# Performance work log

Measured on AMD Instinct MI355X. Metric: run time of the kernel, lower is better.

Reference implementation:

```python
import jax, jax.numpy as jnp
import numpy as np

B, C, H, W = 4, 256, 128, 128


def setup_inputs() -> dict:
    key = jax.random.key(0)
    k1, k2, k3, k4 = jax.random.split(key, 4)
    x = jax.random.normal(k1, (B, C, H, W), dtype=jnp.float32)
    offset = jax.random.normal(k2, (B, 18, H, W), dtype=jnp.float32)
    # 1x1 conv weights, normal_init std=0.01, zero bias (mmcv normal_init default)
    w0 = jax.random.normal(k3, (C, C), dtype=jnp.float32) * 0.01
    b0 = jnp.zeros((C,), dtype=jnp.float32)
    w1 = jax.random.normal(k4, (C, C), dtype=jnp.float32) * 0.01
    b1 = jnp.zeros((C,), dtype=jnp.float32)
    return {"x": x, "offset": offset, "w0": w0, "b0": b0, "w1": w1, "b1": b1}


def _bilinear(x, py, px):
    # x: [B,C,H,W]; py,px: [B,H,W] fractional sample coords; zero outside bounds (DCN convention)
    Bb, Cc, Hh, Ww = x.shape
    y0 = jnp.floor(py)
    x0 = jnp.floor(px)
    wy = (py - y0)[:, None]  # [B,1,H,W]
    wx = (px - x0)[:, None]
    y0i = y0.astype(jnp.int32)
    x0i = x0.astype(jnp.int32)
    xf = x.reshape(Bb, Cc, Hh * Ww)

    def corner(yi, xi):
        valid = ((yi >= 0) & (yi < Hh) & (xi >= 0) & (xi < Ww)).astype(x.dtype)
        idx = (jnp.clip(yi, 0, Hh - 1) * Ww + jnp.clip(xi, 0, Ww - 1)).reshape(Bb, 1, Hh * Ww)
        v = jnp.take_along_axis(xf, idx, axis=2).reshape(Bb, Cc, Hh, Ww)
        return v * valid[:, None]

    v00 = corner(y0i, x0i)
    v01 = corner(y0i, x0i + 1)
    v10 = corner(y0i + 1, x0i)
    v11 = corner(y0i + 1, x0i + 1)
    return (v00 * (1 - wy) * (1 - wx) + v01 * (1 - wy) * wx
            + v10 * wy * (1 - wx) + v11 * wy * wx)


def _channel_norm(t):
    t = t - t.mean(axis=1, keepdims=True)
    return t / jnp.sqrt(jnp.sum(t * t, axis=1, keepdims=True) + 1e-5)


def reference(x, offset, w0, b0, w1, b1):
    Bb, Cc, Hh, Ww = x.shape
    ys = jnp.arange(Hh, dtype=x.dtype)[:, None]  # [H,1]
    xs = jnp.arange(Ww, dtype=x.dtype)[None, :]  # [1,W]
    # deformable 3x3 unfold fused with max over the 9 sample points
    q = None
    for k in range(9):
        kh, kw = k // 3 - 1, k % 3 - 1
        py = ys + kh + offset[:, 2 * k]      # [B,H,W]
        px = xs + kw + offset[:, 2 * k + 1]
        s = _bilinear(x, py, px)             # [B,C,H,W]
        q = s if q is None else jnp.maximum(q, s)
    query = jnp.einsum('oc,bchw->bohw', w0, q) + b0[None, :, None, None]
    key = jnp.einsum('oc,bchw->bohw', w1, x) + b1[None, :, None, None]
    out = jnp.sum(_channel_norm(query) * _channel_norm(key), axis=1, keepdims=True)
    return out  # [B,1,H,W]
```

## Files before the change

kernel.cpp:

```cpp
#include <hip/hip_runtime.h>
#include <math.h>
#include <float.h>

#define Bd 4
#define Cd 256
#define Hd 128
#define Wd 128
#define HW (Hd*Wd)

#define PX 128
#define KC 32
#define PPW 8

#define PXT 64
#define CSTR 264

typedef __attribute__((ext_vector_type(8))) short s16x8;
typedef __attribute__((ext_vector_type(4))) float f32x4;

__device__ __forceinline__ void bf16split(float v, ushort& h, ushort& lo_) {
  uint u = __builtin_bit_cast(uint, v);
  uint uh = u + 0x7FFFu + ((u >> 16) & 1u);
  ushort hh = (ushort)(uh >> 16);
  float hf = __builtin_bit_cast(float, (uint)hh << 16);
  float res = v - hf;
  uint r = __builtin_bit_cast(uint, res);
  uint rl = r + 0x7FFFu + ((r >> 16) & 1u);
  h = hh; lo_ = (ushort)(rl >> 16);
}

__global__ __launch_bounds__(256) void prep_w_k(
    const float* __restrict__ w0, const float* __restrict__ w1,
    ushort* __restrict__ wpk) {
  const int t    = blockIdx.x * 256 + threadIdx.x;
  const int lane = t & 63;
  const int tile = (t >> 6) & 15;
  const int kc   = (t >> 10) & 7;
  const int mat  = t >> 13;
  const float* wsrc = mat ? w1 : w0;
  const int o  = tile * 16 + (lane & 15);
  const int c0 = kc * 32 + (lane >> 4) * 8;
  ushort hi[8], lo[8];
#pragma unroll
  for (int j = 0; j < 8; ++j)
    bf16split(wsrc[o * Cd + c0 + j], hi[j], lo[j]);
  const size_t bh = ((((size_t)(mat * 2 + 0) * 8 + kc) * 16 + tile) * 64 + lane) * 8;
  const size_t bl = ((((size_t)(mat * 2 + 1) * 8 + kc) * 16 + tile) * 64 + lane) * 8;
#pragma unroll
  for (int j = 0; j < 8; ++j) { wpk[bh + j] = hi[j]; wpk[bl + j] = lo[j]; }
}

__global__ __launch_bounds__(256) void transpose_x_k(
    const float* __restrict__ x, float* __restrict__ xT) {
  __shared__ float t[32][33];
  const int b   = blockIdx.z;
  const int hw0 = blockIdx.x * 32;
  const int c0  = blockIdx.y * 32;
  const int tx = threadIdx.x & 31, ty = threadIdx.x >> 5;
  const float* xb  = x  + (size_t)b * Cd * HW;
  float*       xTb = xT + (size_t)b * HW * Cd;
#pragma unroll
  for (int i = 0; i < 32; i += 8)
    t[ty + i][tx] = xb[(size_t)(c0 + ty + i) * HW + hw0 + tx];
  __syncthreads();
#pragma unroll
  for (int i = 0; i < 32; i += 8)
    xTb[(size_t)(hw0 + ty + i) * Cd + c0 + tx] = t[tx][ty + i];
}

__device__ __forceinline__ void deform_job(
    int j, int pbase, const float* __restrict__ offb, uint* __restrict__ dstbase) {
  const int px = j / 9, k = j - px * 9;
  const int p = pbase + px;
  const int h = p >> 7, w = p & (Wd - 1);
  const float oy = offb[(2 * k) * HW + p];
  const float ox = offb[(2 * k + 1) * HW + p];
  const float py = (float)(h + k / 3 - 1) + oy;
  const float pxx = (float)(w + k % 3 - 1) + ox;
  const float y0f = floorf(py), x0f = floorf(pxx);
  const float wy = py - y0f, wx = pxx - x0f;
  const int y0 = (int)y0f, x0 = (int)x0f;
  const int y1 = y0 + 1,  x1 = x0 + 1;
  const float vy0 = (y0 >= 0 && y0 < Hd) ? 1.f : 0.f;
  const float vy1 = (y1 >= 0 && y1 < Hd) ? 1.f : 0.f;
  const float vx0 = (x0 >= 0 && x0 < Wd) ? 1.f : 0.f;
  const float vx1 = (x1 >= 0 && x1 < Wd) ? 1.f : 0.f;
  const int cy0 = min(max(y0, 0), Hd-1), cy1 = min(max(y1, 0), Hd-1);
  const int cx0 = min(max(x0, 0), Wd-1), cx1 = min(max(x1, 0), Wd-1);
  uint4 iv;
  iv.x = (uint)(cy0 * Wd + cx0) * Cd;
  iv.y = (uint)(cy0 * Wd + cx1) * Cd;
  iv.z = (uint)(cy1 * Wd + cx0) * Cd;
  iv.w = (uint)(cy1 * Wd + cx1) * Cd;
  float4 cv;
  cv.x = (1.f-wy)*(1.f-wx) * vy0*vx0;
  cv.y = (1.f-wy)*wx       * vy0*vx1;
  cv.z = wy*(1.f-wx)       * vy1*vx0;
  cv.w = wy*wx             * vy1*vx1;
  uint* d = dstbase + (size_t)(px * 9 + k) * 8;
  *(uint4*)d = iv;
  *(float4*)(d + 4) = cv;
}

__global__ __launch_bounds__(256) void deform_coal_k(
    const float* __restrict__ xT, const float* __restrict__ off,
    float* __restrict__ qT) {
  __shared__ __align__(16) uint coef[4][PPW * 9 * 8];

  const int bid = blockIdx.x;
  const int swz = (bid & 7) * 256 + (bid >> 3);
  const int b    = swz >> 9;
  const int tile = swz & 511;

  const int wv    = threadIdx.x >> 6;
  const int lane  = threadIdx.x & 63;
  const int pbase = (tile * 4 + wv) * PPW;

  const float* offb = off + (size_t)b * 18 * HW;

  deform_job(lane, pbase, offb, &coef[wv][0]);
  if (lane < 8) deform_job(64 + lane, pbase, offb, &coef[wv][0]);
  __syncthreads();

  const float* xTb = xT + (size_t)b * HW * Cd + lane * 4;
  float*       qTb = qT + (size_t)b * HW * Cd + lane * 4;

#pragma unroll 2
  for (int pi = 0; pi < PPW; ++pi) {
    const int p = pbase + pi;
    float m0 = -FLT_MAX, m1 = -FLT_MAX, m2 = -FLT_MAX, m3 = -FLT_MAX;
#pragma unroll
    for (int k = 0; k < 9; ++k) {
      const uint* cp = &coef[wv][(pi * 9 + k) * 8];
      const uint4  iv = *(const uint4*)cp;
      const float4 cw = *(const float4*)(cp + 4);
      const float4 v00 = *(const float4*)(xTb + iv.x);
      const float4 v01 = *(const float4*)(xTb + iv.y);
      const float4 v10 = *(const float4*)(xTb + iv.z);
      const float4 v11 = *(const float4*)(xTb + iv.w);
      m0 = fmaxf(m0, fmaf(cw.x, v00.x, fmaf(cw.y, v01.x, fmaf(cw.z, v10.x, cw.w*v11.x))));
      m1 = fmaxf(m1, fmaf(cw.x, v00.y, fmaf(cw.y, v01.y, fmaf(cw.z, v10.y, cw.w*v11.y))));
      m2 = fmaxf(m2, fmaf(cw.x, v00.z, fmaf(cw.y, v01.z, fmaf(cw.z, v10.z, cw.w*v11.z))));
      m3 = fmaxf(m3, fmaf(cw.x, v00.w, fmaf(cw.y, v01.w, fmaf(cw.z, v10.w, cw.w*v11.w))));
    }
    float4 r; r.x = m0; r.y = m1; r.z = m2; r.w = m3;
    *(float4*)(qTb + (size_t)p * Cd) = r;
  }
}

__global__ __launch_bounds__(512) void fused_mfma_k(
    const float* __restrict__ xT, const float* __restrict__ qT,
    const ushort* __restrict__ wpk,
    const float* __restrict__ b0, const float* __restrict__ b1,
    float* __restrict__ out) {
  __shared__ ushort act[4 * PXT * CSTR];
  const int b   = blockIdx.y;
  const int px0 = blockIdx.x * PXT;
  const int tid = threadIdx.x;
  const int l   = tid & 63, wv = tid >> 6;

  {
    const int r  = tid >> 3;
    const int c0 = (tid & 7) * 32;
    const float* qrow = qT + ((size_t)b * HW + px0 + r) * Cd + c0;
    const float* xrow = xT + ((size_t)b * HW + px0 + r) * Cd + c0;
    ushort* dq_h = act + 0 * PXT * CSTR + r * CSTR + c0;
    ushort* dq_l = act + 1 * PXT * CSTR + r * CSTR + c0;
    ushort* dx_h = act + 2 * PXT * CSTR + r * CSTR + c0;
    ushort* dx_l = act + 3 * PXT * CSTR + r * CSTR + c0;
#pragma unroll
    for (int i = 0; i < 8; ++i) {
      const float4 qv = ((const float4*)qrow)[i];
      const float4 xv = ((const float4*)xrow)[i];
      ushort4 qh, ql, xh, xl;
      bf16split(qv.x, qh.x, ql.x); bf16split(qv.y, qh.y, ql.y);
      bf16split(qv.z, qh.z, ql.z); bf16split(qv.w, qh.w, ql.w);
      bf16split(xv.x, xh.x, xl.x); bf16split(xv.y, xh.y, xl.y);
      bf16split(xv.z, xh.z, xl.z); bf16split(xv.w, xh.w, xl.w);
      *(ushort4*)(dq_h + 4*i) = qh; *(ushort4*)(dq_l + 4*i) = ql;
      *(ushort4*)(dx_h + 4*i) = xh; *(ushort4*)(dx_l + 4*i) = xl;
    }
  }
  __syncthreads();

  const f32x4 z = {0.f, 0.f, 0.f, 0.f};
  f32x4 accQ[2][4], accK[2][4];
#pragma unroll
  for (int a = 0; a < 2; ++a)
#pragma unroll
    for (int bt = 0; bt < 4; ++bt) { accQ[a][bt] = z; accK[a][bt] = z; }

#pragma unroll 2
  for (int kc = 0; kc < 8; ++kc) {
    s16x8 a0h[2], a0l[2], a1h[2], a1l[2];
#pragma unroll
    for (int a = 0; a < 2; ++a) {
      const int tile = wv * 2 + a;
      a0h[a] = *(const s16x8*)(wpk + (((size_t)(0 * 8 + kc) * 16 + tile) * 64 + l) * 8);
      a0l[a] = *(const s16x8*)(wpk + (((size_t)(1 * 8 + kc) * 16 + tile) * 64 + l) * 8);
      a1h[a] = *(const s16x8*)(wpk + (((size_t)(2 * 8 + kc) * 16 + tile) * 64 + l) * 8);
      a1l[a] = *(const s16x8*)(wpk + (((size_t)(3 * 8 + kc) * 16 + tile) * 64 + l) * 8);
    }
#pragma unroll
    for (int bt = 0; bt < 4; ++bt) {
      const int row  = bt * 16 + (l & 15);
      const int coff = kc * 32 + (l >> 4) * 8;
      const ushort* base = act + row * CSTR + coff;
      const s16x8 bqh = *(const s16x8*)(base + 0 * PXT * CSTR);
      const s16x8 bql = *(const s16x8*)(base + 1 * PXT * CSTR);
      const s16x8 bxh = *(const s16x8*)(base + 2 * PXT * CSTR);
      const s16x8 bxl = *(const s16x8*)(base + 3 * PXT * CSTR);
#pragma unroll
      for (int a = 0; a < 2; ++a) {
        accQ[a][bt] = __builtin_amdgcn_mfma_f32_16x16x32_bf16(a0h[a], bqh, accQ[a][bt], 0, 0, 0);
        accQ[a][bt] = __builtin_amdgcn_mfma_f32_16x16x32_bf16(a0h[a], bql, accQ[a][bt], 0, 0, 0);
        accQ[a][bt] = __builtin_amdgcn_mfma_f32_16x16x32_bf16(a0l[a], bqh, accQ[a][bt], 0, 0, 0);
        accK[a][bt] = __builtin_amdgcn_mfma_f32_16x16x32_bf16(a1h[a], bxh, accK[a][bt], 0, 0, 0);
        accK[a][bt] = __builtin_amdgcn_mfma_f32_16x16x32_bf16(a1h[a], bxl, accK[a][bt], 0, 0, 0);
        accK[a][bt] = __builtin_amdgcn_mfma_f32_16x16x32_bf16(a1l[a], bxh, accK[a][bt], 0, 0, 0);
      }
    }
  }

  float bq[2][4], bk[2][4];
#pragma unroll
  for (int a = 0; a < 2; ++a)
#pragma unroll
    for (int r = 0; r < 4; ++r) {
      const int o = wv * 32 + a * 16 + (l >> 4) * 4 + r;
      bq[a][r] = b0[o]; bk[a][r] = b1[o];
    }

  float st[4][5];
#pragma unroll
  for (int bt = 0; bt < 4; ++bt)
#pragma unroll
    for (int s = 0; s < 5; ++s) st[bt][s] = 0.f;
#pragma unroll
  for (int bt = 0; bt < 4; ++bt)
#pragma unroll
    for (int a = 0; a < 2; ++a)
#pragma unroll
      for (int r = 0; r < 4; ++r) {
        const float Qv = accQ[a][bt][r] + bq[a][r];
        const float Kv = accK[a][bt][r] + bk[a][r];
        st[bt][0] += Qv;
        st[bt][1] += Kv;
        st[bt][2] = fmaf(Qv, Qv, st[bt][2]);
        st[bt][3] = fmaf(Kv, Kv, st[bt][3]);
        st[bt][4] = fmaf(Qv, Kv, st[bt][4]);
      }
#pragma unroll
  for (int bt = 0; bt < 4; ++bt)
#pragma unroll
    for (int s = 0; s < 5; ++s) {
      float v = st[bt][s];
      v += __shfl_xor(v, 16, 64);
      v += __shfl_xor(v, 32, 64);
      st[bt][s] = v;
    }

  __syncthreads();
  float* sl = (float*)act;
  {
    const int mybt = l >> 4, col = l & 15;
#pragma unroll
    for (int s = 0; s < 5; ++s)
      sl[((wv * 64) + mybt * 16 + col) * 5 + s] = st[mybt][s];
  }
  __syncthreads();
  if (tid < PXT) {
    float sQ = 0.f, sK = 0.f, sQQ = 0.f, sKK = 0.f, sQK = 0.f;
#pragma unroll
    for (int w8 = 0; w8 < 8; ++w8) {
      const float* p = sl + ((w8 * 64) + tid) * 5;
      sQ += p[0]; sK += p[1]; sQQ += p[2]; sKK += p[3]; sQK += p[4];
    }
    const float num = sQK - sQ * sK * (1.f / 256.f);
    const float dq  = sQQ - sQ * sQ * (1.f / 256.f) + 1e-5f;
    const float dk  = sKK - sK * sK * (1.f / 256.f) + 1e-5f;
    out[(size_t)b * HW + px0 + tid] = num / sqrtf(dq * dk);
  }
}

__global__ __launch_bounds__(256) void transpose_k(
    const float* __restrict__ w0, const float* __restrict__ w1,
    float* __restrict__ w0T, float* __restrict__ w1T) {
  __shared__ float tile[32][33];
  const float* src = blockIdx.y ? w1 : w0;
  float*       dst = blockIdx.y ? w1T : w0T;
  const int bx = blockIdx.x & 7, by = blockIdx.x >> 3;
  const int tx = threadIdx.x & 31, ty = threadIdx.x >> 5;
#pragma unroll
  for (int i = 0; i < 32; i += 8)
    tile[ty + i][tx] = src[(by*32 + ty + i)*Cd + bx*32 + tx];
  __syncthreads();
#pragma unroll
  for (int i = 0; i < 32; i += 8)
    dst[(bx*32 + ty + i)*Cd + by*32 + tx] = tile[tx][ty + i];
}

__global__ __launch_bounds__(256) void deform_max_k(
    const float* __restrict__ x, const float* __restrict__ off,
    float* __restrict__ q) {
  const int b   = blockIdx.y;
  const int c0  = blockIdx.z << 5;
  const int hw0 = (blockIdx.x << 8) + threadIdx.x;
  const int h   = hw0 >> 7;
  const int w   = hw0 & (Wd - 1);
  const float* offb = off + ((size_t)b * 18) * HW + hw0;
  int   i00[9], i01[9], i10[9], i11[9];
  float c00[9], c01[9], c10[9], c11[9];
#pragma unroll
  for (int k = 0; k < 9; ++k) {
    const int kh = k / 3 - 1, kw = k % 3 - 1;
    const float oy = offb[(size_t)(2*k)   * HW];
    const float ox = offb[(size_t)(2*k+1) * HW];
    const float py = (float)(h + kh) + oy;
    const float px = (float)(w + kw) + ox;
    const float y0f = floorf(py), x0f = floorf(px);
    const float wy = py - y0f, wx = px - x0f;
    const int y0 = (int)y0f, x0 = (int)x0f;
    const int y1 = y0 + 1,  x1 = x0 + 1;
    const float vy0 = (y0 >= 0 && y0 < Hd) ? 1.f : 0.f;
    const float vy1 = (y1 >= 0 && y1 < Hd) ? 1.f : 0.f;
    const float vx0 = (x0 >= 0 && x0 < Wd) ? 1.f : 0.f;
    const float vx1 = (x1 >= 0 && x1 < Wd) ? 1.f : 0.f;
    const int cy0 = min(max(y0, 0), Hd-1), cy1 = min(max(y1, 0), Hd-1);
    const int cx0 = min(max(x0, 0), Wd-1), cx1 = min(max(x1, 0), Wd-1);
    i00[k] = cy0 * Wd + cx0;  i01[k] = cy0 * Wd + cx1;
    i10[k] = cy1 * Wd + cx0;  i11[k] = cy1 * Wd + cx1;
    c00[k] = (1.f-wy)*(1.f-wx) * vy0*vx0;
    c01[k] = (1.f-wy)*wx       * vy0*vx1;
    c10[k] = wy*(1.f-wx)       * vy1*vx0;
    c11[k] = wy*wx             * vy1*vx1;
  }
  const float* xb = x + ((size_t)(b * Cd + c0)) * HW;
  float*       qb = q + ((size_t)(b * Cd + c0)) * HW + hw0;
#pragma unroll 4
  for (int c = 0; c < 32; ++c) {
    const float* xc = xb + (size_t)c * HW;
    float m = -3.402823466e38f;
#pragma unroll
    for (int k = 0; k < 9; ++k) {
      const float s = c00[k]*xc[i00[k]] + c01[k]*xc[i01[k]]
                    + c10[k]*xc[i10[k]] + c11[k]*xc[i11[k]];
      m = fmaxf(m, s);
    }
    qb[(size_t)c * HW] = m;
  }
}

__global__ __launch_bounds__(512) void fused_k(
    const float* __restrict__ x, const float* __restrict__ q,
    const float* __restrict__ w0T, const float* __restrict__ w1T,
    const float* __restrict__ b0, const float* __restrict__ b1,
    float* __restrict__ out) {
  __shared__ float w0s[KC * 256];
  __shared__ float w1s[KC * 256];
  __shared__ float qs [KC * PX];
  __shared__ float xs [KC * PX];
  const int b    = blockIdx.y;
  const int px0  = blockIdx.x * PX;
  const int tid  = threadIdx.x;
  const int o_t  = tid & 31;
  const int px_t = tid >> 5;
  float accQ[8][8], accK[8][8];
#pragma unroll
  for (int i = 0; i < 8; ++i) {
    const int o = (i < 4) ? (4*o_t + i) : (128 + 4*o_t + (i - 4));
    const float bqv = b0[o], bkv = b1[o];
#pragma unroll
    for (int j = 0; j < 8; ++j) { accQ[i][j] = bqv; accK[i][j] = bkv; }
  }
  const float* qb = q + ((size_t)b * Cd) * HW + px0;
  const float* xb = x + ((size_t)b * Cd) * HW + px0;
  for (int kc = 0; kc < Cd; kc += KC) {
    __syncthreads();
    {
      const float4* s0 = (const float4*)(w0T + (size_t)kc * 256);
      const float4* s1 = (const float4*)(w1T + (size_t)kc * 256);
      float4* d0 = (float4*)w0s;
      float4* d1 = (float4*)w1s;
#pragma unroll
      for (int i = 0; i < 4; ++i) {
        d0[tid*4 + i] = s0[tid*4 + i];
        d1[tid*4 + i] = s1[tid*4 + i];
      }
#pragma unroll
      for (int i = 0; i < 2; ++i) {
        const int f  = tid*2 + i;
        const int cc = f >> 5, p4 = f & 31;
        ((float4*)qs)[cc*(PX/4) + p4] =
            ((const float4*)(qb + (size_t)(kc+cc) * HW))[p4];
        ((float4*)xs)[cc*(PX/4) + p4] =
            ((const float4*)(xb + (size_t)(kc+cc) * HW))[p4];
      }
    }
    __syncthreads();
#pragma unroll 4
    for (int cc = 0; cc < KC; ++cc) {
      float a0[8], a1[8], qv[8], xv[8];
      *(float4*)&a0[0] = *(const float4*)&w0s[cc*256 + 4*o_t];
      *(float4*)&a0[4] = *(const float4*)&w0s[cc*256 + 128 + 4*o_t];
      *(float4*)&a1[0] = *(const float4*)&w1s[cc*256 + 4*o_t];
      *(float4*)&a1[4] = *(const float4*)&w1s[cc*256 + 128 + 4*o_t];
      *(float4*)&qv[0] = *(const float4*)&qs[cc*PX + 8*px_t];
      *(float4*)&qv[4] = *(const float4*)&qs[cc*PX + 8*px_t + 4];
      *(float4*)&xv[0] = *(const float4*)&xs[cc*PX + 8*px_t];
      *(float4*)&xv[4] = *(const float4*)&xs[cc*PX + 8*px_t + 4];
#pragma unroll
      for (int i = 0; i < 8; ++i)
#pragma unroll
        for (int j = 0; j < 8; ++j) {
          accQ[i][j] = fmaf(a0[i], qv[j], accQ[i][j]);
          accK[i][j] = fmaf(a1[i], xv[j], accK[i][j]);
        }
    }
  }
  float outv[8];
#pragma unroll
  for (int j = 0; j < 8; ++j) {
    float sQ = 0.f, sK = 0.f, sQQ = 0.f, sKK = 0.f, sQK = 0.f;
#pragma unroll
    for (int i = 0; i < 8; ++i) {
      const float Qv = accQ[i][j], Kv = accK[i][j];
      sQ += Qv; sK += Kv;
      sQQ = fmaf(Qv, Qv, sQQ);
      sKK = fmaf(Kv, Kv, sKK);
      sQK = fmaf(Qv, Kv, sQK);
    }
#pragma unroll
    for (int m = 1; m < 32; m <<= 1) {
      sQ  += __shfl_xor(sQ,  m, 64);
      sK  += __shfl_xor(sK,  m, 64);
      sQQ += __shfl_xor(sQQ, m, 64);
      sKK += __shfl_xor(sKK, m, 64);
      sQK += __shfl_xor(sQK, m, 64);
    }
    const float num = sQK - sQ*sK*(1.f/256.f);
    const float dq  = sQQ - sQ*sQ*(1.f/256.f) + 1e-5f;
    const float dk  = sKK - sK*sK*(1.f/256.f) + 1e-5f;
    outv[j] = num / sqrtf(dq * dk);
  }
  if (o_t == 0) {
    float* ob = out + (size_t)b * HW + px0 + px_t*8;
#pragma unroll
    for (int j = 0; j < 8; ++j) ob[j] = outv[j];
  }
}

extern "C" void kernel_launch(void* const* d_in, const int* in_sizes, int n_in,
                              void* d_out, int out_size, void* d_ws, size_t ws_size,
                              hipStream_t stream) {
  const float* x   = (const float*)d_in[0];
  const float* off = (const float*)d_in[1];
  const float* w0  = (const float*)d_in[2];
  const float* b0  = (const float*)d_in[3];
  const float* w1  = (const float*)d_in[4];
  const float* b1  = (const float*)d_in[5];
  float* out = (float*)d_out;

  const size_t tensor_elems = (size_t)Bd * Cd * HW;
  const size_t wpk_bytes    = 4 * 65536 * sizeof(ushort);
  const size_t need_fast    = wpk_bytes + 2 * tensor_elems * 4;

  if (ws_size >= need_fast) {
    ushort* wpk = (ushort*)d_ws;
    float*  xT  = (float*)((char*)d_ws + wpk_bytes);
    float*  qT  = xT + tensor_elems;
    prep_w_k     <<<64, 256, 0, stream>>>(w0, w1, wpk);
    transpose_x_k<<<dim3(HW/32, Cd/32, Bd), 256, 0, stream>>>(x, xT);
    deform_coal_k<<<2048, 256, 0, stream>>>(xT, off, qT);
    fused_mfma_k <<<dim3(HW/PXT, Bd), 512, 0, stream>>>(xT, qT, wpk, b0, b1, out);
  } else {
    float* w0T = (float*)d_ws;
    float* w1T = w0T + 65536;
    float* qws = w1T + 65536;
    transpose_k <<<dim3(64, 2),     256, 0, stream>>>(w0, w1, w0T, w1T);
    deform_max_k<<<dim3(64, Bd, 8), 256, 0, stream>>>(x, off, qws);
    fused_k     <<<dim3(HW/PX, Bd), 512, 0, stream>>>(x, qws, w0T, w1T, b0, b1, out);
  }
}
```

Baseline: 321.0 us.

## Fuse deformable max-sampling into MFMA projection kernel, dropping qT round-trip

Merges the deformable bilinear-max kernel and the MFMA projection/normalization kernel into one kernel. Each 256-thread block handles 32 pixels: it computes the sampled max, splits it to bf16 hi/lo straight into shared memory, then runs the dual 1x1 convs and the channel-norm reduction. This removes writing and re-reading the full qT intermediate through global memory and one kernel launch. In exchange each wave now handles 4 output tiles with fewer pixels per block, so weight fragments are reloaded per 32 pixels instead of per 64, which adds weight traffic and register pressure.

```diff
diff --git a/kernel.cpp b/kernel.cpp
--- a/kernel.cpp
+++ b/kernel.cpp
@@ -10,9 +10,7 @@
 
 #define PX 128
 #define KC 32
-#define PPW 8
-
-#define PXT 64
+#define PXM 32
 #define CSTR 264
 
 typedef __attribute__((ext_vector_type(8))) short s16x8;
@@ -102,116 +100,106 @@
   *(float4*)(d + 4) = cv;
 }
 
-__global__ __launch_bounds__(256) void deform_coal_k(
+__global__ __launch_bounds__(256) void merged_k(
     const float* __restrict__ xT, const float* __restrict__ off,
-    float* __restrict__ qT) {
-  __shared__ __align__(16) uint coef[4][PPW * 9 * 8];
+    const ushort* __restrict__ wpk,
+    const float* __restrict__ b0, const float* __restrict__ b1,
+    float* __restrict__ out) {
+  __shared__ ushort act[4 * PXM * CSTR];
+  __shared__ __align__(16) uint coef[4][8 * 9 * 8];
 
   const int bid = blockIdx.x;
   const int swz = (bid & 7) * 256 + (bid >> 3);
   const int b    = swz >> 9;
   const int tile = swz & 511;
 
-  const int wv    = threadIdx.x >> 6;
-  const int lane  = threadIdx.x & 63;
-  const int pbase = (tile * 4 + wv) * PPW;
-
-  const float* offb = off + (size_t)b * 18 * HW;
-
-  deform_job(lane, pbase, offb, &coef[wv][0]);
-  if (lane < 8) deform_job(64 + lane, pbase, offb, &coef[wv][0]);
-  __syncthreads();
-
-  const float* xTb = xT + (size_t)b * HW * Cd + lane * 4;
-  float*       qTb = qT + (size_t)b * HW * Cd + lane * 4;
-
-#pragma unroll 2
-  for (int pi = 0; pi < PPW; ++pi) {
-    const int p = pbase + pi;
-    float m0 = -FLT_MAX, m1 = -FLT_MAX, m2 = -FLT_MAX, m3 = -FLT_MAX;
-#pragma unroll
-    for (int k = 0; k < 9; ++k) {
-      const uint* cp = &coef[wv][(pi * 9 + k) * 8];
-      const uint4  iv = *(const uint4*)cp;
-      const float4 cw = *(const float4*)(cp + 4);
-      const float4 v00 = *(const float4*)(xTb + iv.x);
-      const float4 v01 = *(const float4*)(xTb + iv.y);
-      const float4 v10 = *(const float4*)(xTb + iv.z);
-      const float4 v11 = *(const float4*)(xTb + iv.w);
-      m0 = fmaxf(m0, fmaf(cw.x, v00.x, fmaf(cw.y, v01.x, fmaf(cw.z, v10.x, cw.w*v11.x))));
-      m1 = fmaxf(m1, fmaf(cw.x, v00.y, fmaf(cw.y, v01.y, fmaf(cw.z, v10.y, cw.w*v11.y))));
-      m2 = fmaxf(m2, fmaf(cw.x, v00.z, fmaf(cw.y, v01.z, fmaf(cw.z, v10.z, cw.w*v11.z))));
-      m3 = fmaxf(m3, fmaf(cw.x, v00.w, fmaf(cw.y, v01.w, fmaf(cw.z, v10.w, cw.w*v11.w))));
-    }
-    float4 r; r.x = m0; r.y = m1; r.z = m2; r.w = m3;
-    *(float4*)(qTb + (size_t)p * Cd) = r;
-  }
-}
-
-__global__ __launch_bounds__(512) void fused_mfma_k(
-    const float* __restrict__ xT, const float* __restrict__ qT,
-    const ushort* __restrict__ wpk,
-    const float* __restrict__ b0, const float* __restrict__ b1,
-    float* __restrict__ out) {
-  __shared__ ushort act[4 * PXT * CSTR];
-  const int b   = blockIdx.y;
-  const int px0 = blockIdx.x * PXT;
   const int tid = threadIdx.x;
   const int l   = tid & 63, wv = tid >> 6;
+  const int px0   = tile * PXM;
+  const int pbase = px0 + wv * 8;
+
+  const float* offb = off + (size_t)b * 18 * HW;
+
+  deform_job(l, pbase, offb, &coef[wv][0]);
+  if (l < 8) deform_job(64 + l, pbase, offb, &coef[wv][0]);
+  __syncthreads();
+
+  {
+    const float* xTb = xT + (size_t)b * HW * Cd + l * 4;
+    ushort* qh_base = act + 0 * PXM * CSTR;
+    ushort* ql_base = act + 1 * PXM * CSTR;
+#pragma unroll 2
+    for (int pi = 0; pi < 8; ++pi) {
+      float m0 = -FLT_MAX, m1 = -FLT_MAX, m2 = -FLT_MAX, m3 = -FLT_MAX;
+#pragma unroll
+      for (int k = 0; k < 9; ++k) {
+        const uint* cp = &coef[wv][(pi * 9 + k) * 8];
+        const uint4  iv = *(const uint4*)cp;
+        const float4 cw = *(const float4*)(cp + 4);
+        const float4 v00 = *(const float4*)(xTb + iv.x);
+        const float4 v01 = *(const float4*)(xTb + iv.y);
+        const float4 v10 = *(const float4*)(xTb + iv.z);
+        const float4 v11 = *(const float4*)(xTb + iv.w);
+        m0 = fmaxf(m0, fmaf(cw.x, v00.x, fmaf(cw.y, v01.x, fmaf(cw.z, v10.x, cw.w*v11.x))));
+        m1 = fmaxf(m1, fmaf(cw.x, v00.y, fmaf(cw.y, v01.y, fmaf(cw.z, v10.y, cw.w*v11.y))));
+        m2 = fmaxf(m2, fmaf(cw.x, v00.z, fmaf(cw.y, v01.z, fmaf(cw.z, v10.z, cw.w*v11.z))));
+        m3 = fmaxf(m3, fmaf(cw.x, v00.w, fmaf(cw.y, v01.w, fmaf(cw.z, v10.w, cw.w*v11.w))));
+      }
+      ushort4 hh, ll;
+      bf16split(m0, hh.x, ll.x); bf16split(m1, hh.y, ll.y);
+      bf16split(m2, hh.z, ll.z); bf16split(m3, hh.w, ll.w);
+      const int pl = wv * 8 + pi;
+      *(ushort4*)(qh_base + pl * CSTR + l * 4) = hh;
+      *(ushort4*)(ql_base + pl * CSTR + l * 4) = ll;
+    }
+  }
 
   {
     const int r  = tid >> 3;
     const int c0 = (tid & 7) * 32;
-    const float* qrow = qT + ((size_t)b * HW + px0 + r) * Cd + c0;
     const float* xrow = xT + ((size_t)b * HW + px0 + r) * Cd + c0;
-    ushort* dq_h = act + 0 * PXT * CSTR + r * CSTR + c0;
-    ushort* dq_l = act + 1 * PXT * CSTR + r * CSTR + c0;
-    ushort* dx_h = act + 2 * PXT * CSTR + r * CSTR + c0;
-    ushort* dx_l = act + 3 * PXT * CSTR + r * CSTR + c0;
+    ushort* dx_h = act + 2 * PXM * CSTR + r * CSTR + c0;
+    ushort* dx_l = act + 3 * PXM * CSTR + r * CSTR + c0;
 #pragma unroll
     for (int i = 0; i < 8; ++i) {
-      const float4 qv = ((const float4*)qrow)[i];
       const float4 xv = ((const float4*)xrow)[i];
-      ushort4 qh, ql, xh, xl;
-      bf16split(qv.x, qh.x, ql.x); bf16split(qv.y, qh.y, ql.y);
-      bf16split(qv.z, qh.z, ql.z); bf16split(qv.w, qh.w, ql.w);
+      ushort4 xh, xl;
       bf16split(xv.x, xh.x, xl.x); bf16split(xv.y, xh.y, xl.y);
       bf16split(xv.z, xh.z, xl.z); bf16split(xv.w, xh.w, xl.w);
-      *(ushort4*)(dq_h + 4*i) = qh; *(ushort4*)(dq_l + 4*i) = ql;
       *(ushort4*)(dx_h + 4*i) = xh; *(ushort4*)(dx_l + 4*i) = xl;
     }
   }
   __syncthreads();
 
   const f32x4 z = {0.f, 0.f, 0.f, 0.f};
-  f32x4 accQ[2][4], accK[2][4];
-#pragma unroll
-  for (int a = 0; a < 2; ++a)
-#pragma unroll
-    for (int bt = 0; bt < 4; ++bt) { accQ[a][bt] = z; accK[a][bt] = z; }
+  f32x4 accQ[4][2], accK[4][2];
+#pragma unroll
+  for (int a = 0; a < 4; ++a)
+#pragma unroll
+    for (int bt = 0; bt < 2; ++bt) { accQ[a][bt] = z; accK[a][bt] = z; }
 
 #pragma unroll 2
   for (int kc = 0; kc < 8; ++kc) {
-    s16x8 a0h[2], a0l[2], a1h[2], a1l[2];
-#pragma unroll
-    for (int a = 0; a < 2; ++a) {
-      const int tile = wv * 2 + a;
-      a0h[a] = *(const s16x8*)(wpk + (((size_t)(0 * 8 + kc) * 16 + tile) * 64 + l) * 8);
-      a0l[a] = *(const s16x8*)(wpk + (((size_t)(1 * 8 + kc) * 16 + tile) * 64 + l) * 8);
-      a1h[a] = *(const s16x8*)(wpk + (((size_t)(2 * 8 + kc) * 16 + tile) * 64 + l) * 8);
-      a1l[a] = *(const s16x8*)(wpk + (((size_t)(3 * 8 + kc) * 16 + tile) * 64 + l) * 8);
-    }
-#pragma unroll
-    for (int bt = 0; bt < 4; ++bt) {
+    s16x8 a0h[4], a0l[4], a1h[4], a1l[4];
+#pragma unroll
+    for (int a = 0; a < 4; ++a) {
+      const int ta = wv * 4 + a;
+      a0h[a] = *(const s16x8*)(wpk + (((size_t)(0 * 8 + kc) * 16 + ta) * 64 + l) * 8);
+      a0l[a] = *(const s16x8*)(wpk + (((size_t)(1 * 8 + kc) * 16 + ta) * 64 + l) * 8);
+      a1h[a] = *(const s16x8*)(wpk + (((size_t)(2 * 8 + kc) * 16 + ta) * 64 + l) * 8);
+      a1l[a] = *(const s16x8*)(wpk + (((size_t)(3 * 8 + kc) * 16 + ta) * 64 + l) * 8);
+    }
+#pragma unroll
+    for (int bt = 0; bt < 2; ++bt) {
       const int row  = bt * 16 + (l & 15);
       const int coff = kc * 32 + (l >> 4) * 8;
       const ushort* base = act + row * CSTR + coff;
-      const s16x8 bqh = *(const s16x8*)(base + 0 * PXT * CSTR);
-      const s16x8 bql = *(const s16x8*)(base + 1 * PXT * CSTR);
-      const s16x8 bxh = *(const s16x8*)(base + 2 * PXT * CSTR);
-      const s16x8 bxl = *(const s16x8*)(base + 3 * PXT * CSTR);
-#pragma unroll
-      for (int a = 0; a < 2; ++a) {
+      const s16x8 bqh = *(const s16x8*)(base + 0 * PXM * CSTR);
+      const s16x8 bql = *(const s16x8*)(base + 1 * PXM * CSTR);
+      const s16x8 bxh = *(const s16x8*)(base + 2 * PXM * CSTR);
+      const s16x8 bxl = *(const s16x8*)(base + 3 * PXM * CSTR);
+#pragma unroll
+      for (int a = 0; a < 4; ++a) {
         accQ[a][bt] = __builtin_amdgcn_mfma_f32_16x16x32_bf16(a0h[a], bqh, accQ[a][bt], 0, 0, 0);
         accQ[a][bt] = __builtin_amdgcn_mfma_f32_16x16x32_bf16(a0h[a], bql, accQ[a][bt], 0, 0, 0);
         accQ[a][bt] = __builtin_amdgcn_mfma_f32_16x16x32_bf16(a0l[a], bqh, accQ[a][bt], 0, 0, 0);
@@ -222,24 +210,24 @@
     }
   }
 
-  float bq[2][4], bk[2][4];
-#pragma unroll
-  for (int a = 0; a < 2; ++a)
+  float bq[4][4], bk[4][4];
+#pragma unroll
+  for (int a = 0; a < 4; ++a)
 #pragma unroll
     for (int r = 0; r < 4; ++r) {
-      const int o = wv * 32 + a * 16 + (l >> 4) * 4 + r;
+      const int o = wv * 64 + a * 16 + (l >> 4) * 4 + r;
       bq[a][r] = b0[o]; bk[a][r] = b1[o];
     }
 
-  float st[4][5];
-#pragma unroll
-  for (int bt = 0; bt < 4; ++bt)
+  float st[2][5];
+#pragma unroll
+  for (int bt = 0; bt < 2; ++bt)
 #pragma unroll
     for (int s = 0; s < 5; ++s) st[bt][s] = 0.f;
 #pragma unroll
-  for (int bt = 0; bt < 4; ++bt)
-#pragma unroll
-    for (int a = 0; a < 2; ++a)
+  for (int bt = 0; bt < 2; ++bt)
+#pragma unroll
+    for (int a = 0; a < 4; ++a)
 #pragma unroll
       for (int r = 0; r < 4; ++r) {
         const float Qv = accQ[a][bt][r] + bq[a][r];
@@ -251,7 +239,7 @@
         st[bt][4] = fmaf(Qv, Kv, st[bt][4]);
       }
 #pragma unroll
-  for (int bt = 0; bt < 4; ++bt)
+  for (int bt = 0; bt < 2; ++bt)
 #pragma unroll
     for (int s = 0; s < 5; ++s) {
       float v = st[bt][s];
@@ -262,18 +250,18 @@
 
   __syncthreads();
   float* sl = (float*)act;
-  {
+  if (l < 32) {
     const int mybt = l >> 4, col = l & 15;
 #pragma unroll
     for (int s = 0; s < 5; ++s)
-      sl[((wv * 64) + mybt * 16 + col) * 5 + s] = st[mybt][s];
-  }
-  __syncthreads();
-  if (tid < PXT) {
+      sl[((wv * 32) + mybt * 16 + col) * 5 + s] = st[mybt][s];
+  }
+  __syncthreads();
+  if (tid < PXM) {
     float sQ = 0.f, sK = 0.f, sQQ = 0.f, sKK = 0.f, sQK = 0.f;
 #pragma unroll
-    for (int w8 = 0; w8 < 8; ++w8) {
-      const float* p = sl + ((w8 * 64) + tid) * 5;
+    for (int w4 = 0; w4 < 4; ++w4) {
+      const float* p = sl + ((w4 * 32) + tid) * 5;
       sQ += p[0]; sK += p[1]; sQQ += p[2]; sKK += p[3]; sQK += p[4];
     }
     const float num = sQK - sQ * sK * (1.f / 256.f);
@@ -463,16 +451,14 @@
 
   const size_t tensor_elems = (size_t)Bd * Cd * HW;
   const size_t wpk_bytes    = 4 * 65536 * sizeof(ushort);
-  const size_t need_fast    = wpk_bytes + 2 * tensor_elems * 4;
+  const size_t need_fast    = wpk_bytes + tensor_elems * 4;
 
   if (ws_size >= need_fast) {
     ushort* wpk = (ushort*)d_ws;
     float*  xT  = (float*)((char*)d_ws + wpk_bytes);
-    float*  qT  = xT + tensor_elems;
     prep_w_k     <<<64, 256, 0, stream>>>(w0, w1, wpk);
     transpose_x_k<<<dim3(HW/32, Cd/32, Bd), 256, 0, stream>>>(x, xT);
-    deform_coal_k<<<2048, 256, 0, stream>>>(xT, off, qT);
-    fused_mfma_k <<<dim3(HW/PXT, Bd), 512, 0, stream>>>(xT, qT, wpk, b0, b1, out);
+    merged_k     <<<2048, 256, 0, stream>>>(xT, off, wpk, b0, b1, out);
   } else {
     float* w0T = (float*)d_ws;
     float* w1T = w0T + 65536;
```

Result: faster. 281.5 us (-12.3%).
